# Kernel tuning notes

Hardware: AMD Instinct MI355X
Metric: run time of the kernel (lower is better)

The kernel has to match this reference:

```python
import jax, jax.numpy as jnp
import numpy as np

N_CLASS = 5      # episode way
SHOTS = 5        # support images per class
D = 64           # local descriptor dim (feature_dim)
H = W = 16       # feature map spatial size
N_QUERY = 75     # 15 queries per class


def setup_inputs() -> dict:
    key = jax.random.key(0)
    k1, k2 = jax.random.split(key)
    support = jax.random.normal(k1, (N_CLASS * SHOTS, D, H, W), dtype=jnp.float32)
    query = jax.random.normal(k2, (N_QUERY, D, H, W), dtype=jnp.float32)
    return {"support": support, "query": query, "task_index": 0, "k": 3, "k2": 64}


def reference(support, query, task_index, k, k2):
    C = N_CLASS
    n, d, h, w = support.shape
    hw = h * w
    ns = n // C  # shots per class

    # Per-class support descriptors: [C, ns*h*w, d], L2-normalized along d
    s = support.reshape(C, ns, d, hw)
    s = jnp.transpose(s, (0, 1, 3, 2)).reshape(C, ns * hw, d)
    s = s / jnp.linalg.norm(s, axis=-1, keepdims=True)

    # Query local descriptors: [B, d, Nq], L2-normalized along d
    B = query.shape[0]
    q = query.reshape(B, d, -1)
    q = q / jnp.linalg.norm(q, axis=1, keepdims=True)

    # Cosine similarity per class: [C, B, Nq, M]  (M = ns*h*w support descriptors)
    sim = jnp.einsum('cmd,bdq->cbqm', s, q)

    # torch.topk(sim, k, dim=1): top-k over support descriptors M per query location
    v = jax.lax.top_k(sim, k)[0]          # [C, B, Nq, k]
    v = jnp.swapaxes(v, 2, 3)             # [C, B, k, Nq]
    # torch.topk(., k2, dim=2): top-k2 over query locations
    v = jax.lax.top_k(v, k2)[0]           # [C, B, k, k2]

    # cat over classes, unsqueeze, then view(-1, 1, k, k2)
    return v.reshape(-1, 1, k, k2)        # [C*B, 1, k, k2]
```

## Files before the change

### kernel.cpp

```cpp
#include <hip/hip_runtime.h>
#include <stdint.h>


#define C_CLS 5
#define SHOTS 5
#define DIM 64
#define HW 256
#define NQ 75
#define K1 3
#define K2 64
#define M_TOT 1280
#define MQ 4
#define NSTEP 20
#define QG 4

using bf16x8 = __attribute__((ext_vector_type(8))) short;
using u32x4  = __attribute__((ext_vector_type(4))) unsigned int;
using f32x4  = __attribute__((ext_vector_type(4))) float;

__device__ inline unsigned short f2bf(float x) {
    uint32_t u = __float_as_uint(x);
    u += 0x7FFF + ((u >> 16) & 1);
    return (unsigned short)(u >> 16);
}

__device__ __forceinline__ void ins3(float v, float& t0, float& t1, float& t2) {
    t2 = __builtin_amdgcn_fmed3f(v, t1, t2);
    t1 = __builtin_amdgcn_fmed3f(v, t0, t1);
    t0 = fmaxf(t0, v);
}

__global__ __launch_bounds__(256)
void prep(const float* __restrict__ support, const float* __restrict__ query,
          unsigned short* __restrict__ Sn, unsigned short* __restrict__ Qn) {
    const int tid  = threadIdx.x;
    const int wv   = tid >> 6, lane = tid & 63;
    const int dg   = lane >> 4, dl = lane & 15;
    const int bid  = blockIdx.x;
    const float* src;
    unsigned short* dstblk;
    if (bid < NQ * 4) {
        const int b    = bid >> 2;
        const int desc = (bid & 3) * 64 + wv * 16 + dl;
        src    = query + (size_t)b * DIM * HW + desc;
        dstblk = Qn + (size_t)b * 16384 + (size_t)((bid & 3) * 4 + wv) * 1024;
    } else {
        const int sb   = bid - NQ * 4;
        const int cs   = sb >> 2;
        const int desc = (sb & 3) * 64 + wv * 16 + dl;
        const int c = cs / SHOTS, s = cs % SHOTS;
        src    = support + (size_t)cs * DIM * HW + desc;
        dstblk = Sn + (size_t)c * 81920 + (size_t)(s * 16 + (sb & 3) * 4 + wv) * 1024;
    }
    float v[16];
    float nrm = 0.f;
#pragma unroll
    for (int i = 0; i < 16; ++i) {
        const float x = src[(dg * 16 + i) * HW];
        v[i] = x; nrm = fmaf(x, x, nrm);
    }
    nrm += __shfl_xor(nrm, 16, 64);
    nrm += __shfl_xor(nrm, 32, 64);
    const float inv = rsqrtf(nrm);
    uint32_t p[8];
#pragma unroll
    for (int j = 0; j < 8; ++j)
        p[j] = (uint32_t)f2bf(v[2 * j] * inv) | ((uint32_t)f2bf(v[2 * j + 1] * inv) << 16);
    const int ck = dg >> 1;
#pragma unroll
    for (int q = 0; q < 2; ++q) {
        const int kg = (dg & 1) * 2 + q;
        uint4 wq = {p[q * 4 + 0], p[q * 4 + 1], p[q * 4 + 2], p[q * 4 + 3]};
        *(uint4*)(dstblk + ck * 512 + (kg * 16 + dl) * 8) = wq;
    }
}

__global__ __launch_bounds__(256)
void dn4_mfma(const unsigned short* __restrict__ Sn,
              const unsigned short* __restrict__ Qn,
              unsigned short* __restrict__ partial) {
    const int tid  = threadIdx.x;
    const int lane = tid & 63, w = tid >> 6;
    const int c15  = lane & 15, kg = lane >> 4;
    const int bid  = blockIdx.x;
    const int b    = bid % NQ;
    const int cq   = bid / NQ;
    const int c    = cq >> 2, qt = cq & 3;

    bf16x8 aq[QG][2];
    const unsigned short* qf = Qn + (size_t)b * 16384 + (size_t)(w * QG) * 1024;
#pragma unroll
    for (int g = 0; g < QG; ++g)
#pragma unroll
        for (int ck = 0; ck < 2; ++ck)
            aq[g][ck] = __builtin_bit_cast(bf16x8,
                *(const u32x4*)(qf + g * 1024 + ck * 512 + lane * 8));

    float t0[QG][4], t1[QG][4], t2[QG][4];
#pragma unroll
    for (int g = 0; g < QG; ++g)
#pragma unroll
        for (int r = 0; r < 4; ++r) { t0[g][r] = -2.f; t1[g][r] = -2.f; t2[g][r] = -2.f; }

    const f32x4 Z = {0.f, 0.f, 0.f, 0.f};
    const unsigned short* sp = Sn + (size_t)c * 81920 + (size_t)qt * (NSTEP * 1024);

    u32x4 p0 = *(const u32x4*)(sp + lane * 8);
    u32x4 p1 = *(const u32x4*)(sp + 512 + lane * 8);
#pragma unroll
    for (int it = 0; it < NSTEP; ++it) {
        u32x4 n0 = p0, n1 = p1;
        if (it + 1 < NSTEP) {
            const unsigned short* rp = sp + (it + 1) * 1024 + lane * 8;
            n0 = *(const u32x4*)rp;
            n1 = *(const u32x4*)(rp + 512);
        }
        const bf16x8 b0 = __builtin_bit_cast(bf16x8, p0);
        const bf16x8 b1 = __builtin_bit_cast(bf16x8, p1);
#pragma unroll
        for (int g = 0; g < QG; ++g) {
            f32x4 acc = __builtin_amdgcn_mfma_f32_16x16x32_bf16(aq[g][0], b0, Z, 0, 0, 0);
            acc = __builtin_amdgcn_mfma_f32_16x16x32_bf16(aq[g][1], b1, acc, 0, 0, 0);
#pragma unroll
            for (int r = 0; r < 4; ++r)
                ins3(acc[r], t0[g][r], t1[g][r], t2[g][r]);
        }
        p0 = n0; p1 = n1;
    }

#pragma unroll
    for (int g = 0; g < QG; ++g)
#pragma unroll
        for (int r = 0; r < 4; ++r)
#pragma unroll
            for (int off = 1; off < 16; off <<= 1) {
                const float o0 = __shfl_xor(t0[g][r], off, 64);
                const float o1 = __shfl_xor(t1[g][r], off, 64);
                const float o2 = __shfl_xor(t2[g][r], off, 64);
                const float x = fmaxf(t0[g][r], o2);
                const float y = fmaxf(t1[g][r], o1);
                const float z = fmaxf(t2[g][r], o0);
                t0[g][r] = fmaxf(fmaxf(x, y), z);
                t1[g][r] = __builtin_amdgcn_fmed3f(x, y, z);
                t2[g][r] = fminf(fminf(x, y), z);
            }

    if (c15 == 0) {
        unsigned short* pbase =
            partial + (((size_t)(c * NQ + b) * MQ + qt) * K1) * HW;
#pragma unroll
        for (int g = 0; g < QG; ++g)
#pragma unroll
            for (int r = 0; r < 4; ++r) {
                const int qloc = (w * QG + g) * 16 + kg * 4 + r;
                pbase[qloc]          = f2bf(t0[g][r]);
                pbase[HW + qloc]     = f2bf(t1[g][r]);
                pbase[2 * HW + qloc] = f2bf(t2[g][r]);
            }
    }
}

__global__ __launch_bounds__(256)
void dn4_topq(const unsigned short* __restrict__ partial, float* __restrict__ out) {
    __shared__ float sbuf[HW];
    const int tid = threadIdx.x;
    const int bid = blockIdx.x;
    const int ki  = bid % K1;
    const int cb  = bid / K1;

    const unsigned short* p = partial + (size_t)cb * MQ * K1 * HW + tid;
    float t0 = -2.f, t1 = -2.f, t2 = -2.f;
#pragma unroll
    for (int h = 0; h < MQ; ++h)
#pragma unroll
        for (int r = 0; r < K1; ++r) {
            const float v = __uint_as_float((uint32_t)p[(h * K1 + r) * HW] << 16);
            ins3(v, t0, t1, t2);
        }
    float v = (ki == 0) ? t0 : (ki == 1) ? t1 : t2;

#pragma unroll
    for (int kk = 2; kk <= HW; kk <<= 1) {
#pragma unroll
        for (int j = kk >> 1; j > 0; j >>= 1) {
            const bool keep_max = (((tid & kk) == 0) == ((tid & j) == 0));
            float wv;
            if (j >= 64) {
                sbuf[tid] = v;
                __syncthreads();
                wv = sbuf[tid ^ j];
                __syncthreads();
            } else {
                wv = __shfl_xor(v, j, 64);
            }
            v = keep_max ? fmaxf(v, wv) : fminf(v, wv);
        }
    }
    if (tid < K2) out[(size_t)cb * K1 * K2 + (size_t)ki * K2 + tid] = v;
}

extern "C" void kernel_launch(void* const* d_in, const int* in_sizes, int n_in,
                              void* d_out, int out_size, void* d_ws, size_t ws_size,
                              hipStream_t stream) {
    const float* support = (const float*)d_in[0];
    const float* query   = (const float*)d_in[1];
    float* out = (float*)d_out;

    char* ws = (char*)d_ws;
    unsigned short* Sn      = (unsigned short*)ws;
    unsigned short* Qn      = (unsigned short*)(ws + 819200);
    unsigned short* partial = (unsigned short*)(ws + 819200 + 2457600);

    prep    <<<dim3(400),              dim3(256), 0, stream>>>(support, query, Sn, Qn);
    dn4_mfma<<<dim3(C_CLS * MQ * NQ),  dim3(256), 0, stream>>>(Sn, Qn, partial);
    dn4_topq<<<dim3(C_CLS * NQ * K1),  dim3(256), 0, stream>>>(partial, out);
}
```

Before: 51.25 us.

## Stage support tiles in LDS via global_load_lds with doubled block size

Expands the similarity kernel to 512 threads, so each wave handles 2 query groups instead of 4. Support tiles are now staged cooperatively into a double-buffered LDS area with direct global-to-LDS loads and shared by all 8 waves. Previously each wave streamed the same support data from global memory into registers on its own. This cuts redundant global/L2 traffic and raises wave count, at the cost of a barrier per iteration and LDS reads.

```diff
diff --git a/kernel.cpp b/kernel.cpp
--- a/kernel.cpp
+++ b/kernel.cpp
@@ -11,12 +11,19 @@
 #define K2 64
 #define M_TOT 1280
 #define MQ 4
-#define NSTEP 20
-#define QG 4
+#define NIT 5
+#define QG 2
 
 using bf16x8 = __attribute__((ext_vector_type(8))) short;
 using u32x4  = __attribute__((ext_vector_type(4))) unsigned int;
 using f32x4  = __attribute__((ext_vector_type(4))) float;
+
+typedef __attribute__((address_space(1))) const unsigned int GU32;
+typedef __attribute__((address_space(3))) unsigned int LU32;
+
+__device__ __forceinline__ void gload16(const void* g, void* l) {
+    __builtin_amdgcn_global_load_lds((GU32*)g, (LU32*)l, 16, 0, 0);
+}
 
 __device__ inline unsigned short f2bf(float x) {
     uint32_t u = __float_as_uint(x);
@@ -75,10 +82,12 @@
     }
 }
 
-__global__ __launch_bounds__(256)
+__global__ __launch_bounds__(512)
 void dn4_mfma(const unsigned short* __restrict__ Sn,
               const unsigned short* __restrict__ Qn,
               unsigned short* __restrict__ partial) {
+    __shared__ unsigned short sB[2][4 * 1024];
+
     const int tid  = threadIdx.x;
     const int lane = tid & 63, w = tid >> 6;
     const int c15  = lane & 15, kg = lane >> 4;
@@ -103,29 +112,33 @@
         for (int r = 0; r < 4; ++r) { t0[g][r] = -2.f; t1[g][r] = -2.f; t2[g][r] = -2.f; }
 
     const f32x4 Z = {0.f, 0.f, 0.f, 0.f};
-    const unsigned short* sp = Sn + (size_t)c * 81920 + (size_t)qt * (NSTEP * 1024);
-
-    u32x4 p0 = *(const u32x4*)(sp + lane * 8);
-    u32x4 p1 = *(const u32x4*)(sp + 512 + lane * 8);
-#pragma unroll
-    for (int it = 0; it < NSTEP; ++it) {
-        u32x4 n0 = p0, n1 = p1;
-        if (it + 1 < NSTEP) {
-            const unsigned short* rp = sp + (it + 1) * 1024 + lane * 8;
-            n0 = *(const u32x4*)rp;
-            n1 = *(const u32x4*)(rp + 512);
-        }
-        const bf16x8 b0 = __builtin_bit_cast(bf16x8, p0);
-        const bf16x8 b1 = __builtin_bit_cast(bf16x8, p1);
-#pragma unroll
-        for (int g = 0; g < QG; ++g) {
-            f32x4 acc = __builtin_amdgcn_mfma_f32_16x16x32_bf16(aq[g][0], b0, Z, 0, 0, 0);
-            acc = __builtin_amdgcn_mfma_f32_16x16x32_bf16(aq[g][1], b1, acc, 0, 0, 0);
-#pragma unroll
-            for (int r = 0; r < 4; ++r)
-                ins3(acc[r], t0[g][r], t1[g][r], t2[g][r]);
-        }
-        p0 = n0; p1 = n1;
+    const char* tb0 = (const char*)Sn + (size_t)c * 163840 + (size_t)qt * 40960;
+
+    gload16(tb0 + tid * 16, (char*)sB[0] + w * 1024);
+    __syncthreads();
+
+    int cur = 0;
+    for (int it = 0; it < NIT; ++it) {
+        if (it < NIT - 1) {
+            const char* tb = tb0 + (size_t)(it + 1) * 8192;
+            gload16(tb + tid * 16, (char*)sB[cur ^ 1] + w * 1024);
+        }
+#pragma unroll
+        for (int ns = 0; ns < 4; ++ns) {
+            const unsigned short* rp = &sB[cur][ns * 1024 + lane * 8];
+            const bf16x8 b0 = __builtin_bit_cast(bf16x8, *(const u32x4*)rp);
+            const bf16x8 b1 = __builtin_bit_cast(bf16x8, *(const u32x4*)(rp + 512));
+#pragma unroll
+            for (int g = 0; g < QG; ++g) {
+                f32x4 acc = __builtin_amdgcn_mfma_f32_16x16x32_bf16(aq[g][0], b0, Z, 0, 0, 0);
+                acc = __builtin_amdgcn_mfma_f32_16x16x32_bf16(aq[g][1], b1, acc, 0, 0, 0);
+#pragma unroll
+                for (int r = 0; r < 4; ++r)
+                    ins3(acc[r], t0[g][r], t1[g][r], t2[g][r]);
+            }
+        }
+        __syncthreads();
+        cur ^= 1;
     }
 
 #pragma unroll
@@ -212,6 +225,6 @@
     unsigned short* partial = (unsigned short*)(ws + 819200 + 2457600);
 
     prep    <<<dim3(400),              dim3(256), 0, stream>>>(support, query, Sn, Qn);
-    dn4_mfma<<<dim3(C_CLS * MQ * NQ),  dim3(256), 0, stream>>>(Sn, Qn, partial);
+    dn4_mfma<<<dim3(C_CLS * MQ * NQ),  dim3(512), 0, stream>>>(Sn, Qn, partial);
     dn4_topq<<<dim3(C_CLS * NQ * K1),  dim3(256), 0, stream>>>(partial, out);
 }
```

Measured after the change: 49.70 us. 1.03x faster.
